# Performance work log

Hardware: AMD Instinct MI355X
Metric: run time of the kernel (lower is better)

The kernel has to match this reference:

```python
import jax, jax.numpy as jnp
import numpy as np
from jax.scipy.special import gammaln

MAX_POS = 4096
NUM_HEADS = 8
TEMP = 1.0        # gumbel-sigmoid (RelaxedBernoulli) temperature
THRESHOLD = 0.5   # hard-boundary threshold
PRIOR = 0.2       # binomial prior on boundary rate


def setup_inputs() -> dict:
    key = jax.random.key(0)
    ks = jax.random.split(key, 6)
    B, S, D = 8, 4096, 1024
    lim = (6.0 / (D + D)) ** 0.5  # xavier_uniform for square [D,D] weights
    return {
        "hidden": jax.random.normal(ks[0], (B, S, D), jnp.float32),
        "pos_emb": 0.02 * jax.random.normal(ks[1], (MAX_POS, D), jnp.float32),
        "Wq": jax.random.uniform(ks[2], (D, D), jnp.float32, -lim, lim),
        "Wk": jax.random.uniform(ks[3], (D, D), jnp.float32, -lim, lim),
        "sig_temp": jnp.ones((1,), jnp.float32),    # sigmoid_temperature param
        "sig_thr": jnp.zeros((1,), jnp.float32),    # sigmoid_threshold param
        "noise_u": jax.random.uniform(ks[4], (B, S), jnp.float32),
    }


def reference(hidden, pos_emb, Wq, Wk, sig_temp, sig_thr, noise_u):
    B, S, D = hidden.shape
    scale = (D // NUM_HEADS) ** -0.5
    dt = hidden.dtype

    # add positional embeddings, then L2-normalize (F.normalize eps=1e-12)
    h = hidden + pos_emb[:S][None]
    h = h / jnp.maximum(jnp.linalg.norm(h, axis=-1, keepdims=True), 1e-12)

    Q = h @ Wq.T  # [B,S,D]
    K = h @ Wk.T  # [B,S,D]

    # full QK^T masked to only (i, i-1) survivors + row-sum == adjacent dots
    adj = jnp.einsum('bsd,bsd->bs', Q[:, 1:], K[:, :-1]) * scale  # [B,S-1]
    boundary_scores = jnp.concatenate([jnp.zeros((B, 1), dt), adj], axis=1)

    probs = jax.nn.sigmoid((boundary_scores - sig_thr) / sig_temp)
    probs = jnp.clip(probs, 0.0, 1.0)
    probs = probs.at[:, 0].set(1.0)

    # RelaxedBernoulli rsample (torch clamp_probs uses finfo.eps)
    eps = jnp.finfo(dt).eps
    p = jnp.clip(probs, eps, 1.0 - eps)
    logits = jnp.log(p) - jnp.log1p(-p)
    u = jnp.clip(noise_u, eps, 1.0 - eps)
    logistic = jnp.log(u) - jnp.log1p(-u)
    soft = jax.nn.sigmoid((logits + logistic) / TEMP)

    # straight-through hard boundaries
    hard = (soft > THRESHOLD).astype(dt)
    hard = jax.lax.stop_gradient(hard - soft) + soft

    # delete(hard_boundaries, hidden): segment mean-pooling between boundaries,
    # padded to S segments (jit-static shape)
    seg = jnp.clip(jnp.cumsum(hard, axis=1).astype(jnp.int32) - 1, 0, S - 1)  # [B,S]
    sums = jax.vmap(lambda ids, x: jax.ops.segment_sum(x, ids, num_segments=S))(seg, h)
    cnts = jax.vmap(lambda ids: jax.ops.segment_sum(jnp.ones((S,), dt), ids, num_segments=S))(seg)
    pooled = sums / jnp.maximum(cnts, 1.0)[..., None]  # [B,S,D]
    pooled = jnp.transpose(pooled, (1, 0, 2))          # [S,B,D]

    # binomial prior loss on boundary counts
    n = jnp.asarray(S, dt)
    k = jnp.sum(hard, axis=-1)
    log_prob = (gammaln(n + 1.0) - gammaln(k + 1.0) - gammaln(n - k + 1.0)
                + k * jnp.log(PRIOR) + (n - k) * jnp.log1p(-PRIOR))
    loss = -jnp.mean(log_prob) / n
    return pooled, loss
```

## Files before the change

### kernel.cpp

```cpp
#include <hip/hip_runtime.h>
#include <stdint.h>

namespace {

constexpr int Bb = 8, S = 4096, D = 1024, BS = 32768;
constexpr float SCALE = 0.08838834764831845f;
constexpr float FEPS  = 1.1920928955078125e-07f;
constexpr int MAXF = 4096;

typedef unsigned short u16;
typedef __attribute__((ext_vector_type(8))) _Float16 f16x8;
typedef __attribute__((ext_vector_type(4))) float    f32x4;

__device__ __forceinline__ u16 f2h(float f) {
  _Float16 h = (_Float16)f;
  return __builtin_bit_cast(u16, h);
}
__device__ __forceinline__ float h2f(u16 u) {
  return (float)__builtin_bit_cast(_Float16, u);
}
__device__ __forceinline__ void gload_lds16(const void* g, void* l) {
  __builtin_amdgcn_global_load_lds((const __attribute__((address_space(1))) void*)g,
                                   (__attribute__((address_space(3))) void*)l, 16, 0, 0);
}
#define VMCNT(n) asm volatile("s_waitcnt vmcnt(" #n ")" ::: "memory")

__global__ void prep_h(const float* __restrict__ hidden, const float* __restrict__ pos,
                       u16* __restrict__ Hf, int* __restrict__ fcnt) {
  if (blockIdx.x == 0 && threadIdx.x == 0) *fcnt = 0;
  const int r = blockIdx.x;
  const int t = threadIdx.x;
  const float4 hv = ((const float4*)(hidden + (size_t)r * D))[t];
  const float4 pv = ((const float4*)(pos + (size_t)(r & (S - 1)) * D))[t];
  float x0 = hv.x + pv.x, x1 = hv.y + pv.y, x2 = hv.z + pv.z, x3 = hv.w + pv.w;
  float ss = x0 * x0 + x1 * x1 + x2 * x2 + x3 * x3;
  #pragma unroll
  for (int m = 1; m < 64; m <<= 1) ss += __shfl_xor(ss, m, 64);
  __shared__ float red[4];
  if ((t & 63) == 0) red[t >> 6] = ss;
  __syncthreads();
  const float nrm = fmaxf(sqrtf(red[0] + red[1] + red[2] + red[3]), 1e-12f);
  ((ushort4*)(Hf + (size_t)r * D))[t] = make_ushort4(
      f2h(x0 / nrm), f2h(x1 / nrm), f2h(x2 / nrm), f2h(x3 / nrm));
}

__global__ void gemm_G_part(const float* __restrict__ Wq, const float* __restrict__ Wk,
                            float* __restrict__ Gpart) {
  __shared__ float Qs[32][64];
  __shared__ float Ks[32][64];
  const int t = threadIdx.x;
  const int i0 = blockIdx.x * 64, j0 = blockIdx.y * 64;
  const int kz = blockIdx.z * 256;
  const int tx = t & 15, ty = t >> 4;
  float acc[4][4] = {};
  for (int k0 = kz; k0 < kz + 256; k0 += 32) {
    #pragma unroll
    for (int q = 0; q < 2; ++q) {
      const int c = t + q * 256;
      const int row = c >> 4, c4 = (c & 15) << 2;
      *(float4*)&Qs[row][c4] = *(const float4*)&Wq[(size_t)(k0 + row) * D + i0 + c4];
      *(float4*)&Ks[row][c4] = *(const float4*)&Wk[(size_t)(k0 + row) * D + j0 + c4];
    }
    __syncthreads();
    #pragma unroll 8
    for (int kk = 0; kk < 32; ++kk) {
      const float4 qa = *(const float4*)&Qs[kk][tx << 2];
      const float4 kb = *(const float4*)&Ks[kk][ty << 2];
      const float qq[4] = {qa.x, qa.y, qa.z, qa.w};
      const float kv[4] = {kb.x, kb.y, kb.z, kb.w};
      #pragma unroll
      for (int a = 0; a < 4; ++a)
        #pragma unroll
        for (int bj = 0; bj < 4; ++bj) acc[a][bj] = fmaf(qq[a], kv[bj], acc[a][bj]);
    }
    __syncthreads();
  }
  float* gp = Gpart + (size_t)blockIdx.z * 1048576;
  #pragma unroll
  for (int a = 0; a < 4; ++a) {
    const int i = i0 + (tx << 2) + a;
    *(float4*)&gp[(size_t)i * D + j0 + (ty << 2)] =
        make_float4(acc[a][0], acc[a][1], acc[a][2], acc[a][3]);
  }
}

__global__ void gemm_G_comb(const float* __restrict__ Gpart,
                            float* __restrict__ Gf32, u16* __restrict__ Gf16) {
  const size_t e = ((size_t)blockIdx.x * 256 + threadIdx.x) * 4;
  float4 a = *(const float4*)&Gpart[e];
  #pragma unroll
  for (int z = 1; z < 4; ++z) {
    const float4 p = *(const float4*)&Gpart[(size_t)z * 1048576 + e];
    a.x += p.x; a.y += p.y; a.z += p.z; a.w += p.w;
  }
  *(float4*)&Gf32[e] = a;
  *(ushort4*)&Gf16[e] = make_ushort4(f2h(a.x), f2h(a.y), f2h(a.z), f2h(a.w));
}

__global__ __launch_bounds__(512, 2) void gemm_main(
    const u16* __restrict__ Hf, const u16* __restrict__ Gf,
    float* __restrict__ adj_part) {
  __shared__ u16 Abuf[2][16384];
  __shared__ u16 Bbuf[2][16384];
  __shared__ float adjp[4][256];

  const int tid = threadIdx.x;
  const int bid = blockIdx.x;
  const int swz = (bid & 7) * 64 + (bid >> 3);
  const int mt = swz >> 2, nt = swz & 3;
  const int r0 = mt << 8;
  const int n0g = nt << 8;

  const int wave = tid >> 6, lane = tid & 63;
  const int wr = wave >> 2;
  const int wc = wave & 3;
  const int frow = lane & 15;
  const int fgrp = lane >> 4;
  const int sw = (lane & 7) << 4;
  const int cb0 = (fgrp * 16) ^ sw;
  const int cb1 = (64 + fgrp * 16) ^ sw;
  const int Abase = (wr * 128 + frow) * 128;
  const int Bbase = (wc * 64 + frow) * 128;

  const int trow = tid >> 3;
  const int scb = ((tid & 7) << 4) ^ ((trow & 7) << 4);
  const char* Asrc = (const char*)Hf + (size_t)(r0 + trow) * 2048 + scb;
  const char* Bsrc = (const char*)Gf + (size_t)(n0g + trow) * 2048 + scb;
  const int dst16 = tid * 16;

  f32x4 acc[8][4];
  #pragma unroll
  for (int m = 0; m < 8; ++m)
    #pragma unroll
    for (int n = 0; n < 4; ++n) acc[m][n] = (f32x4){0.f, 0.f, 0.f, 0.f};

  auto stage = [&](int b, int kt) {
    #pragma unroll
    for (int q = 0; q < 4; ++q) {
      gload_lds16(Asrc + (size_t)q * 131072 + (size_t)kt * 128,
                  (char*)&Abuf[b][0] + q * 8192 + dst16);
      gload_lds16(Bsrc + (size_t)q * 131072 + (size_t)kt * 128,
                  (char*)&Bbuf[b][0] + q * 8192 + dst16);
    }
  };

  auto compute = [&](int b) {
    const char* Ab = (const char*)&Abuf[b][0];
    const char* Bp = (const char*)&Bbuf[b][0];
    #pragma unroll
    for (int ks = 0; ks < 2; ++ks) {
      const int cb = ks ? cb1 : cb0;
      f16x8 bf[4], af[8];
      #pragma unroll
      for (int n = 0; n < 4; ++n) bf[n] = *(const f16x8*)(Bp + Bbase + n * 2048 + cb);
      #pragma unroll
      for (int m = 0; m < 8; ++m) af[m] = *(const f16x8*)(Ab + Abase + m * 2048 + cb);
      __builtin_amdgcn_s_setprio(1);
      #pragma unroll
      for (int m = 0; m < 8; ++m)
        #pragma unroll
        for (int n = 0; n < 4; ++n)
          acc[m][n] = __builtin_amdgcn_mfma_f32_16x16x32_f16(af[m], bf[n], acc[m][n], 0, 0, 0);
      __builtin_amdgcn_s_setprio(0);
    }
  };

  stage(0, 0);
  #pragma unroll 1
  for (int t = 0; t < 16; ++t) {
    VMCNT(0);
    __builtin_amdgcn_s_barrier();
    __builtin_amdgcn_sched_barrier(0);
    if (t < 15) stage((t + 1) & 1, t + 1);
    __builtin_amdgcn_sched_barrier(0);
    compute(t & 1);
  }

  #pragma unroll
  for (int m = 0; m < 8; ++m) {
    #pragma unroll
    for (int reg = 0; reg < 4; ++reg) {
      const int rl = wr * 128 + m * 16 + fgrp * 4 + reg;
      const int gr = r0 + rl;
      float sum = 0.f;
      if (((gr + 1) & (S - 1)) != 0) {
        const u16* hrow = Hf + (size_t)(gr + 1) * D + n0g + wc * 64 + frow;
        #pragma unroll
        for (int n = 0; n < 4; ++n)
          sum = fmaf(acc[m][n][reg], h2f(hrow[n * 16]), sum);
      }
      #pragma unroll
      for (int off = 1; off < 16; off <<= 1) sum += __shfl_xor(sum, off, 64);
      if (frow == 0) adjp[wc][rl] = sum;
    }
  }
  __syncthreads();
  if (tid < 256) {
    adj_part[(size_t)nt * BS + r0 + tid] =
        adjp[0][tid] + adjp[1][tid] + adjp[2][tid] + adjp[3][tid];
  }
}

__global__ void score_flag(const float* __restrict__ adj_part,
                           const float* __restrict__ sig_temp, const float* __restrict__ sig_thr,
                           const float* __restrict__ noise_u,
                           unsigned char* __restrict__ hard, int* __restrict__ flags,
                           int* __restrict__ fcnt) {
  const int idx = blockIdx.x * 256 + threadIdx.x;
  const int s = idx & (S - 1);
  float sc = 0.f;
  if (s > 0) {
    float a = 0.f;
    #pragma unroll
    for (int p = 0; p < 4; ++p) a += adj_part[(size_t)p * BS + idx - 1];
    sc = a * SCALE;
  }
  const float temp = sig_temp[0], thr = sig_thr[0];
  float pr = 1.f / (1.f + expf(-(sc - thr) / temp));
  pr = fminf(fmaxf(pr, 0.f), 1.f);
  if (s == 0) pr = 1.f;
  const float p = fminf(fmaxf(pr, FEPS), 1.f - FEPS);
  const float lgt = logf(p) - log1pf(-p);
  const float uu = fminf(fmaxf(noise_u[idx], FEPS), 1.f - FEPS);
  const float lgs = logf(uu) - log1pf(-uu);
  const float z = lgt + lgs;
  hard[idx] = (z > 0.f) ? 1 : 0;
  if (s > 0 && fabsf(z) < 1e-3f) {
    const int k = atomicAdd(fcnt, 1);
    if (k < MAXF) flags[k] = idx;
  }
}

__global__ __launch_bounds__(256) void fixup_part(const int* __restrict__ flags,
    const int* __restrict__ fcnt, const float* __restrict__ hidden,
    const float* __restrict__ pos, const float* __restrict__ Gf32,
    float* __restrict__ pz) {
  __shared__ float h0s[1024];
  __shared__ float h1s[1024];
  __shared__ float red[4];
  const int t = threadIdx.x;
  const int slice = blockIdx.x & 7;
  const int nf = min(*fcnt, MAXF);
  for (int w = blockIdx.x >> 3; w < nf; w += 32) {
    const int idx = flags[w];
    #pragma unroll
    for (int rr = 0; rr < 2; ++rr) {
      const int r = idx - 1 + rr;
      float* hs = rr ? h1s : h0s;
      const float4 hv = ((const float4*)(hidden + (size_t)r * D))[t];
      const float4 pv = ((const float4*)(pos + (size_t)(r & (S - 1)) * D))[t];
      const float x0 = hv.x + pv.x, x1 = hv.y + pv.y, x2 = hv.z + pv.z, x3 = hv.w + pv.w;
      float ss = x0 * x0 + x1 * x1 + x2 * x2 + x3 * x3;
      #pragma unroll
      for (int m = 1; m < 64; m <<= 1) ss += __shfl_xor(ss, m, 64);
      __syncthreads();
      if ((t & 63) == 0) red[t >> 6] = ss;
      __syncthreads();
      const float nrm = fmaxf(sqrtf(red[0] + red[1] + red[2] + red[3]), 1e-12f);
      hs[4 * t + 0] = x0 / nrm; hs[4 * t + 1] = x1 / nrm;
      hs[4 * t + 2] = x2 / nrm; hs[4 * t + 3] = x3 / nrm;
    }
    __syncthreads();
    const float4 h0v = *(const float4*)&h0s[t << 2];
    float acc = 0.f;
    const int i0 = slice << 7;
    #pragma unroll 4
    for (int i = i0; i < i0 + 128; ++i) {
      const float4 g = ((const float4*)(Gf32 + (size_t)i * D))[t];
      const float d = g.x * h0v.x + g.y * h0v.y + g.z * h0v.z + g.w * h0v.w;
      acc = fmaf(h1s[i], d, acc);
    }
    #pragma unroll
    for (int m = 1; m < 64; m <<= 1) acc += __shfl_xor(acc, m, 64);
    __syncthreads();
    if ((t & 63) == 0) red[t >> 6] = acc;
    __syncthreads();
    if (t == 0) pz[(size_t)w * 8 + slice] = red[0] + red[1] + red[2] + red[3];
    __syncthreads();
  }
}

__global__ void fixup_final(const int* __restrict__ flags, const int* __restrict__ fcnt,
    const float* __restrict__ pz,
    const float* __restrict__ sig_temp, const float* __restrict__ sig_thr,
    const float* __restrict__ noise_u, unsigned char* __restrict__ hard) {
  const int w = blockIdx.x * 256 + threadIdx.x;
  const int nf = min(*fcnt, MAXF);
  if (w >= nf) return;
  const int idx = flags[w];
  float a = 0.f;
  #pragma unroll
  for (int p = 0; p < 8; ++p) a += pz[(size_t)w * 8 + p];
  const float sc = a * SCALE;
  const float temp = sig_temp[0], thr = sig_thr[0];
  float pr = 1.f / (1.f + expf(-(sc - thr) / temp));
  pr = fminf(fmaxf(pr, 0.f), 1.f);
  const float p = fminf(fmaxf(pr, FEPS), 1.f - FEPS);
  const float lgt = logf(p) - log1pf(-p);
  const float uu = fminf(fmaxf(noise_u[idx], FEPS), 1.f - FEPS);
  const float lgs = logf(uu) - log1pf(-uu);
  hard[idx] = ((lgt + lgs) > 0.f) ? 1 : 0;
}

__global__ void decide_scan(const unsigned char* __restrict__ hard_,
                            int* __restrict__ seg_start, int* __restrict__ nseg_out,
                            float* __restrict__ kf_out) {
  const int b = blockIdx.x, t = threadIdx.x;
  __shared__ int ssum[256];
  const uint4 hv = ((const uint4*)(hard_ + (size_t)b * S))[t];
  const uint32_t wds[4] = {hv.x, hv.y, hv.z, hv.w};
  const uint32_t bsum = hv.x + hv.y + hv.z + hv.w;
  const int loc = (int)((bsum & 255) + ((bsum >> 8) & 255) +
                        ((bsum >> 16) & 255) + (bsum >> 24));
  ssum[t] = loc;
  __syncthreads();
  for (int off = 1; off < 256; off <<= 1) {
    int v = ssum[t];
    if (t >= off) v += ssum[t - off];
    __syncthreads();
    ssum[t] = v;
    __syncthreads();
  }
  const int ktot = ssum[255];
  int cum = ssum[t] - loc;
  #pragma unroll
  for (int e = 0; e < 16; ++e) {
    const int s = (t << 4) + e;
    const int bit = (int)((wds[e >> 2] >> ((e & 3) * 8)) & 1);
    const int pseg = min(max(cum - 1, 0), S - 1);
    cum += bit;
    const int seg = min(max(cum - 1, 0), S - 1);
    if (s == 0 || seg != pseg) seg_start[b * S + seg] = s;
  }
  if (t == 0) {
    nseg_out[b] = min(max(ktot, 1), S);
    kf_out[b] = (float)ktot;
  }
}

__global__ void pool(const u16* __restrict__ Hf,
                     const int* __restrict__ seg_start, const int* __restrict__ nseg_arr,
                     float* __restrict__ out) {
  const int j = blockIdx.x, b = blockIdx.y, t = threadIdx.x;
  const int ns = nseg_arr[b];
  float4* o = (float4*)(out + (((size_t)j * Bb + b) << 10));
  if (j >= ns) {
    o[t] = (float4){0.f, 0.f, 0.f, 0.f};
    return;
  }
  const int s0 = seg_start[b * S + j];
  const int s1 = (j + 1 < ns) ? seg_start[b * S + j + 1] : S;
  float a0 = 0.f, a1 = 0.f, a2 = 0.f, a3 = 0.f;
  for (int s = s0; s < s1; ++s) {
    const ushort4 hv = *(const ushort4*)(Hf + (((size_t)b * S + s) << 10) + (t << 2));
    a0 += h2f(hv.x); a1 += h2f(hv.y); a2 += h2f(hv.z); a3 += h2f(hv.w);
  }
  const float c = (float)(s1 - s0);
  o[t] = (float4){a0 / c, a1 / c, a2 / c, a3 / c};
}

__global__ void loss_k(const float* __restrict__ kf, float* __restrict__ out) {
  const int t = threadIdx.x;
  float lp = 0.f;
  if (t < 8) {
    const float n = 4096.f;
    const float k = kf[t];
    lp = lgammaf(n + 1.f) - lgammaf(k + 1.f) - lgammaf(n - k + 1.f)
       + k * logf(0.2f) + (n - k) * log1pf(-0.2f);
  }
  #pragma unroll
  for (int off = 1; off < 8; off <<= 1) lp += __shfl_xor(lp, off, 64);
  if (t == 0) out[(size_t)BS * 1024] = -(lp / 8.f) / 4096.f;
}

}

extern "C" void kernel_launch(void* const* d_in, const int* in_sizes, int n_in,
                              void* d_out, int out_size, void* d_ws, size_t ws_size,
                              hipStream_t stream) {
  (void)in_sizes; (void)n_in; (void)out_size; (void)ws_size;
  const float* hidden = (const float*)d_in[0];
  const float* pos    = (const float*)d_in[1];
  const float* Wq     = (const float*)d_in[2];
  const float* Wk     = (const float*)d_in[3];
  const float* stemp  = (const float*)d_in[4];
  const float* sthr   = (const float*)d_in[5];
  const float* nois   = (const float*)d_in[6];
  float* out = (float*)d_out;
  char* ws = (char*)d_ws;

  u16*   Hf        = (u16*)(ws);
  u16*   Gf16      = (u16*)(ws + 67108864);
  float* Gf32      = (float*)(ws + 69206016);
  float* adj_part  = (float*)(ws + 73400320);
  unsigned char* hard = (unsigned char*)(ws + 74448896);
  int*   flags     = (int*)(ws + 74481664);
  float* pz        = (float*)(ws + 74498048);
  int*   fcnt      = (int*)(ws + 74629120);
  int*   seg_start = (int*)(ws + 74629184);
  int*   nseg      = (int*)(ws + 74760256);
  float* kf        = (float*)(ws + 74760320);
  float* Gpart     = (float*)(ws + 74760384);

  hipLaunchKernelGGL(prep_h,      dim3(BS),         dim3(256), 0, stream, hidden, pos, Hf, fcnt);
  hipLaunchKernelGGL(gemm_G_part, dim3(16, 16, 4),  dim3(256), 0, stream, Wq, Wk, Gpart);
  hipLaunchKernelGGL(gemm_G_comb, dim3(1024),       dim3(256), 0, stream, Gpart, Gf32, Gf16);
  hipLaunchKernelGGL(gemm_main,   dim3(512),        dim3(512), 0, stream, Hf, Gf16, adj_part);
  hipLaunchKernelGGL(score_flag,  dim3(BS/256),     dim3(256), 0, stream, adj_part, stemp, sthr, nois, hard, flags, fcnt);
  hipLaunchKernelGGL(fixup_part,  dim3(256),        dim3(256), 0, stream, flags, fcnt, hidden, pos, Gf32, pz);
  hipLaunchKernelGGL(fixup_final, dim3(MAXF/256),   dim3(256), 0, stream, flags, fcnt, pz, stemp, sthr, nois, hard);
  hipLaunchKernelGGL(decide_scan, dim3(Bb),         dim3(256), 0, stream, hard, seg_start, nseg, kf);
  hipLaunchKernelGGL(pool,        dim3(S, Bb),      dim3(256), 0, stream, Hf, seg_start, nseg, out);
  hipLaunchKernelGGL(loss_k,      dim3(1),          dim3(64),  0, stream, kf, out);
}
```

Before: 236.4 us.

## Split GEMM k-tile into four phases interleaving partial loads with MFMA

The main GEMM loop is restructured so each k-tile is processed in four sub-phases. Each phase reads a quarter of the A fragments from LDS, issues a slice of the next tile's global-to-LDS loads, and runs 16 MFMAs, with fine-grained vmcnt waits replacing one full drain per tile. LDS staging is remapped so rows are loaded in per-phase groups. The intent is to hide global load latency behind MFMA work and shrink register pressure for A fragments, at the cost of more barriers per iteration and tricky vmcnt bookkeeping.

```diff
diff --git a/kernel.cpp b/kernel.cpp
--- a/kernel.cpp
+++ b/kernel.cpp
@@ -24,6 +24,7 @@
                                    (__attribute__((address_space(3))) void*)l, 16, 0, 0);
 }
 #define VMCNT(n) asm volatile("s_waitcnt vmcnt(" #n ")" ::: "memory")
+#define LGKM0 asm volatile("s_waitcnt lgkmcnt(0)" ::: "memory")
 
 __global__ void prep_h(const float* __restrict__ hidden, const float* __restrict__ pos,
                        u16* __restrict__ Hf, int* __restrict__ fcnt) {
@@ -119,14 +120,16 @@
   const int sw = (lane & 7) << 4;
   const int cb0 = (fgrp * 16) ^ sw;
   const int cb1 = (64 + fgrp * 16) ^ sw;
-  const int Abase = (wr * 128 + frow) * 128;
-  const int Bbase = (wc * 64 + frow) * 128;
-
-  const int trow = tid >> 3;
-  const int scb = ((tid & 7) << 4) ^ ((trow & 7) << 4);
-  const char* Asrc = (const char*)Hf + (size_t)(r0 + trow) * 2048 + scb;
-  const char* Bsrc = (const char*)Gf + (size_t)(n0g + trow) * 2048 + scb;
-  const int dst16 = tid * 16;
+  const int ABrow = wr * 128 + frow;
+  const int Brow = wc * 64 + frow;
+
+  const int subrow = tid >> 3;
+  const int chunk = tid & 7;
+  const int scb = (chunk << 4) ^ ((subrow & 7) << 4);
+  const char* HfB = (const char*)Hf;
+  const char* GfB = (const char*)Gf;
+  char* AbB = (char*)&Abuf[0][0];
+  char* BbB = (char*)&Bbuf[0][0];
 
   f32x4 acc[8][4];
   #pragma unroll
@@ -134,46 +137,104 @@
     #pragma unroll
     for (int n = 0; n < 4; ++n) acc[m][n] = (f32x4){0.f, 0.f, 0.f, 0.f};
 
-  auto stage = [&](int b, int kt) {
-    #pragma unroll
-    for (int q = 0; q < 4; ++q) {
-      gload_lds16(Asrc + (size_t)q * 131072 + (size_t)kt * 128,
-                  (char*)&Abuf[b][0] + q * 8192 + dst16);
-      gload_lds16(Bsrc + (size_t)q * 131072 + (size_t)kt * 128,
-                  (char*)&Bbuf[b][0] + q * 8192 + dst16);
-    }
+  auto stAq = [&](char* dst, int kt, int q) {
+    const int row = 32 * q + (subrow & 31) + ((subrow >> 5) << 7);
+    gload_lds16(HfB + (size_t)(r0 + row) * 2048 + (size_t)kt * 128 + scb,
+                dst + row * 128 + (chunk << 4));
   };
-
-  auto compute = [&](int b) {
-    const char* Ab = (const char*)&Abuf[b][0];
-    const char* Bp = (const char*)&Bbuf[b][0];
-    #pragma unroll
-    for (int ks = 0; ks < 2; ++ks) {
-      const int cb = ks ? cb1 : cb0;
-      f16x8 bf[4], af[8];
-      #pragma unroll
-      for (int n = 0; n < 4; ++n) bf[n] = *(const f16x8*)(Bp + Bbase + n * 2048 + cb);
-      #pragma unroll
-      for (int m = 0; m < 8; ++m) af[m] = *(const f16x8*)(Ab + Abase + m * 2048 + cb);
-      __builtin_amdgcn_s_setprio(1);
-      #pragma unroll
-      for (int m = 0; m < 8; ++m)
-        #pragma unroll
-        for (int n = 0; n < 4; ++n)
-          acc[m][n] = __builtin_amdgcn_mfma_f32_16x16x32_f16(af[m], bf[n], acc[m][n], 0, 0, 0);
-      __builtin_amdgcn_s_setprio(0);
+  auto stBh = [&](char* dst, int kt, int u) {
+    {
+      const int rb = subrow;
+      const int cr = ((rb >> 5) << 6) + (rb & 31) + (u << 5);
+      gload_lds16(GfB + (size_t)(n0g + cr) * 2048 + (size_t)kt * 128 + scb,
+                  dst + cr * 128 + (chunk << 4));
+    }
+    {
+      const int rb = 64 + subrow;
+      const int cr = ((rb >> 5) << 6) + (rb & 31) + (u << 5);
+      gload_lds16(GfB + (size_t)(n0g + cr) * 2048 + (size_t)kt * 128 + scb,
+                  dst + cr * 128 + (chunk << 4));
     }
   };
 
-  stage(0, 0);
+  f16x8 a[2][2], b[4][2];
+
+#define READ_A(Q) \
+  a[0][0] = *(const f16x8*)(Ac + (ABrow + (2*(Q)) * 16) * 128 + cb0); \
+  a[0][1] = *(const f16x8*)(Ac + (ABrow + (2*(Q)) * 16) * 128 + cb1); \
+  a[1][0] = *(const f16x8*)(Ac + (ABrow + (2*(Q)+1) * 16) * 128 + cb0); \
+  a[1][1] = *(const f16x8*)(Ac + (ABrow + (2*(Q)+1) * 16) * 128 + cb1);
+
+#define MFMA8(MI, Q) \
+  acc[2*(Q)+(MI)][0] = __builtin_amdgcn_mfma_f32_16x16x32_f16(a[MI][0], b[0][0], acc[2*(Q)+(MI)][0], 0, 0, 0); \
+  acc[2*(Q)+(MI)][0] = __builtin_amdgcn_mfma_f32_16x16x32_f16(a[MI][1], b[0][1], acc[2*(Q)+(MI)][0], 0, 0, 0); \
+  acc[2*(Q)+(MI)][1] = __builtin_amdgcn_mfma_f32_16x16x32_f16(a[MI][0], b[1][0], acc[2*(Q)+(MI)][1], 0, 0, 0); \
+  acc[2*(Q)+(MI)][1] = __builtin_amdgcn_mfma_f32_16x16x32_f16(a[MI][1], b[1][1], acc[2*(Q)+(MI)][1], 0, 0, 0); \
+  acc[2*(Q)+(MI)][2] = __builtin_amdgcn_mfma_f32_16x16x32_f16(a[MI][0], b[2][0], acc[2*(Q)+(MI)][2], 0, 0, 0); \
+  acc[2*(Q)+(MI)][2] = __builtin_amdgcn_mfma_f32_16x16x32_f16(a[MI][1], b[2][1], acc[2*(Q)+(MI)][2], 0, 0, 0); \
+  acc[2*(Q)+(MI)][3] = __builtin_amdgcn_mfma_f32_16x16x32_f16(a[MI][0], b[3][0], acc[2*(Q)+(MI)][3], 0, 0, 0); \
+  acc[2*(Q)+(MI)][3] = __builtin_amdgcn_mfma_f32_16x16x32_f16(a[MI][1], b[3][1], acc[2*(Q)+(MI)][3], 0, 0, 0);
+
+#define SB __builtin_amdgcn_sched_barrier(0)
+#define BAR __builtin_amdgcn_s_barrier()
+
+  stBh(BbB, 0, 0);
+  stBh(BbB, 0, 1);
+  stAq(AbB, 0, 0); stAq(AbB, 0, 1); stAq(AbB, 0, 2); stAq(AbB, 0, 3);
+
   #pragma unroll 1
   for (int t = 0; t < 16; ++t) {
-    VMCNT(0);
-    __builtin_amdgcn_s_barrier();
-    __builtin_amdgcn_sched_barrier(0);
-    if (t < 15) stage((t + 1) & 1, t + 1);
-    __builtin_amdgcn_sched_barrier(0);
-    compute(t & 1);
+    const int cs = t & 1;
+    char* Ac = AbB + (size_t)cs * 32768;
+    char* Bc = BbB + (size_t)cs * 32768;
+    char* An = AbB + (size_t)(cs ^ 1) * 32768;
+    char* Bn = BbB + (size_t)(cs ^ 1) * 32768;
+    const bool hn = (t < 15);
+
+    VMCNT(3);
+    BAR;
+    READ_A(0);
+    #pragma unroll
+    for (int n = 0; n < 4; ++n) {
+      b[n][0] = *(const f16x8*)(Bc + (Brow + n * 16) * 128 + cb0);
+      b[n][1] = *(const f16x8*)(Bc + (Brow + n * 16) * 128 + cb1);
+    }
+    if (hn) stBh(Bn, t + 1, 0);
+    BAR;
+    LGKM0; SB;
+    __builtin_amdgcn_s_setprio(1);
+    MFMA8(0, 0) MFMA8(1, 0)
+    __builtin_amdgcn_s_setprio(0);
+
+    if (hn) { VMCNT(4); } else { VMCNT(2); }
+    BAR;
+    READ_A(1);
+    if (hn) stBh(Bn, t + 1, 1);
+    BAR;
+    LGKM0; SB;
+    __builtin_amdgcn_s_setprio(1);
+    MFMA8(0, 1) MFMA8(1, 1)
+    __builtin_amdgcn_s_setprio(0);
+
+    if (hn) { VMCNT(5); } else { VMCNT(1); }
+    BAR;
+    READ_A(2);
+    if (hn) { stAq(An, t + 1, 0); stAq(An, t + 1, 1); }
+    BAR;
+    LGKM0; SB;
+    __builtin_amdgcn_s_setprio(1);
+    MFMA8(0, 2) MFMA8(1, 2)
+    __builtin_amdgcn_s_setprio(0);
+
+    if (hn) { VMCNT(6); } else { VMCNT(0); }
+    BAR;
+    READ_A(3);
+    if (hn) { stAq(An, t + 1, 2); stAq(An, t + 1, 3); }
+    BAR;
+    LGKM0; SB;
+    __builtin_amdgcn_s_setprio(1);
+    MFMA8(0, 3) MFMA8(1, 3)
+    __builtin_amdgcn_s_setprio(0);
   }
 
   #pragma unroll
@@ -199,6 +260,10 @@
     adj_part[(size_t)nt * BS + r0 + tid] =
         adjp[0][tid] + adjp[1][tid] + adjp[2][tid] + adjp[3][tid];
   }
+#undef READ_A
+#undef MFMA8
+#undef SB
+#undef BAR
 }
 
 __global__ void score_flag(const float* __restrict__ adj_part,
```

Measured after the change: 232.8 us. No clear change (-1.5%).

## Load GEMM B operand straight into registers and double-buffer it

Applied to the files above, without the earlier changes.

Removes the shared-memory staging buffer for the G (B) operand in gemm_main. Each wave now loads its B fragments directly from global memory into a register double buffer one k-tile ahead. A is still staged through LDS. The old full vmcnt(0) drain is replaced with a partial vmcnt(8) wait, and the two k-substeps are split so the A fragment loads for the second half overlap with the MFMAs of the first. The aim is to cut LDS traffic and footprint and to overlap loads with compute better. The cost is more register pressure and redundant, less coalesced global/L2 reads of B across waves.

```diff
diff --git a/kernel.cpp b/kernel.cpp
--- a/kernel.cpp
+++ b/kernel.cpp
@@ -101,7 +101,6 @@
     const u16* __restrict__ Hf, const u16* __restrict__ Gf,
     float* __restrict__ adj_part) {
   __shared__ u16 Abuf[2][16384];
-  __shared__ u16 Bbuf[2][16384];
   __shared__ float adjp[4][256];
 
   const int tid = threadIdx.x;
@@ -119,14 +118,15 @@
   const int sw = (lane & 7) << 4;
   const int cb0 = (fgrp * 16) ^ sw;
   const int cb1 = (64 + fgrp * 16) ^ sw;
-  const int Abase = (wr * 128 + frow) * 128;
-  const int Bbase = (wc * 64 + frow) * 128;
-
-  const int trow = tid >> 3;
-  const int scb = ((tid & 7) << 4) ^ ((trow & 7) << 4);
-  const char* Asrc = (const char*)Hf + (size_t)(r0 + trow) * 2048 + scb;
-  const char* Bsrc = (const char*)Gf + (size_t)(n0g + trow) * 2048 + scb;
-  const int dst16 = tid * 16;
+  const int ABrow = wr * 128 + frow;
+
+  const int subrow = tid >> 3;
+  const int chunk = tid & 7;
+  const int scb = (chunk << 4) ^ ((subrow & 7) << 4);
+  const char* HfB = (const char*)Hf;
+  char* AbB = (char*)&Abuf[0][0];
+
+  const u16* Bbase = Gf + (size_t)(n0g + wc * 64 + frow) * 1024 + fgrp * 8;
 
   f32x4 acc[8][4];
   #pragma unroll
@@ -134,46 +134,63 @@
     #pragma unroll
     for (int n = 0; n < 4; ++n) acc[m][n] = (f32x4){0.f, 0.f, 0.f, 0.f};
 
-  auto stage = [&](int b, int kt) {
+  auto stageA = [&](char* dst, int kt) {
     #pragma unroll
     for (int q = 0; q < 4; ++q) {
-      gload_lds16(Asrc + (size_t)q * 131072 + (size_t)kt * 128,
-                  (char*)&Abuf[b][0] + q * 8192 + dst16);
-      gload_lds16(Bsrc + (size_t)q * 131072 + (size_t)kt * 128,
-                  (char*)&Bbuf[b][0] + q * 8192 + dst16);
+      const int row = (q << 6) + subrow;
+      gload_lds16(HfB + (size_t)(r0 + row) * 2048 + (size_t)kt * 128 + scb,
+                  dst + row * 128 + (chunk << 4));
     }
   };
-
-  auto compute = [&](int b) {
-    const char* Ab = (const char*)&Abuf[b][0];
-    const char* Bp = (const char*)&Bbuf[b][0];
-    #pragma unroll
-    for (int ks = 0; ks < 2; ++ks) {
-      const int cb = ks ? cb1 : cb0;
-      f16x8 bf[4], af[8];
-      #pragma unroll
-      for (int n = 0; n < 4; ++n) bf[n] = *(const f16x8*)(Bp + Bbase + n * 2048 + cb);
-      #pragma unroll
-      for (int m = 0; m < 8; ++m) af[m] = *(const f16x8*)(Ab + Abase + m * 2048 + cb);
-      __builtin_amdgcn_s_setprio(1);
-      #pragma unroll
-      for (int m = 0; m < 8; ++m)
-        #pragma unroll
-        for (int n = 0; n < 4; ++n)
-          acc[m][n] = __builtin_amdgcn_mfma_f32_16x16x32_f16(af[m], bf[n], acc[m][n], 0, 0, 0);
-      __builtin_amdgcn_s_setprio(0);
-    }
+  auto loadB = [&](f16x8 (&Bd)[4][2], int kt) {
+    #pragma unroll
+    for (int n = 0; n < 4; ++n)
+      #pragma unroll
+      for (int ks = 0; ks < 2; ++ks)
+        Bd[n][ks] = *(const f16x8*)(Bbase + (size_t)n * 16384 + kt * 64 + ks * 32);
   };
 
-  stage(0, 0);
+  f16x8 BP[4][2], BQ[4][2];
+
+  auto TILE = [&](f16x8 (&Bcur)[4][2], f16x8 (&Bnext)[4][2], int cs, int t, bool doNext) {
+    VMCNT(8);
+    __builtin_amdgcn_s_barrier();
+    const char* Ac = AbB + cs * 32768;
+    char* An = AbB + (cs ^ 1) * 32768;
+    f16x8 a0[8];
+    #pragma unroll
+    for (int m = 0; m < 8; ++m)
+      a0[m] = *(const f16x8*)(Ac + (ABrow + m * 16) * 128 + cb0);
+    if (doNext) { stageA(An, t + 1); loadB(Bnext, t + 1); }
+    __builtin_amdgcn_sched_barrier(0);
+    __builtin_amdgcn_s_setprio(1);
+    #pragma unroll
+    for (int m = 0; m < 8; ++m)
+      #pragma unroll
+      for (int n = 0; n < 4; ++n)
+        acc[m][n] = __builtin_amdgcn_mfma_f32_16x16x32_f16(a0[m], Bcur[n][0], acc[m][n], 0, 0, 0);
+    __builtin_amdgcn_s_setprio(0);
+    f16x8 a1[8];
+    #pragma unroll
+    for (int m = 0; m < 8; ++m)
+      a1[m] = *(const f16x8*)(Ac + (ABrow + m * 16) * 128 + cb1);
+    __builtin_amdgcn_s_setprio(1);
+    #pragma unroll
+    for (int m = 0; m < 8; ++m)
+      #pragma unroll
+      for (int n = 0; n < 4; ++n)
+        acc[m][n] = __builtin_amdgcn_mfma_f32_16x16x32_f16(a1[m], Bcur[n][1], acc[m][n], 0, 0, 0);
+    __builtin_amdgcn_s_setprio(0);
+    __builtin_amdgcn_sched_barrier(0);
+  };
+
+  stageA(AbB, 0);
+  loadB(BP, 0);
+
   #pragma unroll 1
-  for (int t = 0; t < 16; ++t) {
-    VMCNT(0);
-    __builtin_amdgcn_s_barrier();
-    __builtin_amdgcn_sched_barrier(0);
-    if (t < 15) stage((t + 1) & 1, t + 1);
-    __builtin_amdgcn_sched_barrier(0);
-    compute(t & 1);
+  for (int it = 0; it < 8; ++it) {
+    TILE(BP, BQ, 0, 2 * it, true);
+    TILE(BQ, BP, 1, 2 * it + 1, it < 7);
   }
 
   #pragma unroll
```

Result: slower. 418.8 us (+77.2%).
